# Performance work log

Measured on AMD Instinct MI355X. Metric: run time of the kernel, lower is better.

The kernel has to match this reference:

```python
import jax, jax.numpy as jnp
import numpy as np
from jax import lax

BASE_SIZE = 16.0
FEAT_STRIDE = 16
RATIOS = (0.5, 1.0, 2.0)
SCALES = (8.0, 16.0, 32.0)
N_PRE_NMS = 6000   # eval-mode ProposalCreator defaults
N_POST_NMS = 300
NMS_THRESH = 0.7
MIN_SIZE = 16.0
SCALE = 1.0


def anchor_base():
    # generate_anchor_base: loops ratio-major, scale-minor -> 9 anchors (y1,x1,y2,x2)
    r = jnp.asarray(RATIOS, jnp.float32)
    s = jnp.asarray(SCALES, jnp.float32)
    h = (BASE_SIZE * s[None, :] * jnp.sqrt(r)[:, None]).reshape(-1)
    w = (BASE_SIZE * s[None, :] * jnp.sqrt(1.0 / r)[:, None]).reshape(-1)
    c = BASE_SIZE / 2.0
    return jnp.stack([c - h / 2, c - w / 2, c + h / 2, c + w / 2], axis=1)  # [9,4]


def enumerate_anchors(hh, ww):
    # replicates _enumerate_shift_anchor incl. torch.meshgrid(shift_x, shift_y) 'ij' ordering
    sy = jnp.arange(hh, dtype=jnp.float32) * FEAT_STRIDE
    sx = jnp.arange(ww, dtype=jnp.float32) * FEAT_STRIDE
    gx, gy = jnp.meshgrid(sx, sy, indexing='ij')  # shapes [ww, hh]
    shift = jnp.stack([gy.ravel(), gx.ravel(), gy.ravel(), gx.ravel()], axis=1)  # [K,4]
    a = anchor_base()[None, :, :] + shift[:, None, :]  # [K,9,4]
    return a.reshape(-1, 4)


def conv2d(x, w, b, pad):
    y = lax.conv_general_dilated(x, w, (1, 1), [(pad, pad), (pad, pad)],
                                 dimension_numbers=('NCHW', 'OIHW', 'NCHW'))
    return y + b[None, :, None, None]


def loc2bbox(anchor, loc):
    h = anchor[:, 2] - anchor[:, 0]
    w = anchor[:, 3] - anchor[:, 1]
    cy = anchor[:, 0] + 0.5 * h
    cx = anchor[:, 1] + 0.5 * w
    dy, dx, dh, dw = loc[:, 0], loc[:, 1], loc[:, 2], loc[:, 3]
    cy = dy * h + cy
    cx = dx * w + cx
    h = jnp.exp(dh) * h
    w = jnp.exp(dw) * w
    return jnp.stack([cy - 0.5 * h, cx - 0.5 * w, cy + 0.5 * h, cx + 0.5 * w], axis=1)


def propose(loc, score, anchor, img_h, img_w):
    # ProposalCreator for a single image: decode, clip, min-size filter, top-k, NMS, pad to N_POST_NMS
    roi = loc2bbox(anchor, loc)
    roi = jnp.stack([jnp.clip(roi[:, 0], 0.0, img_h), jnp.clip(roi[:, 1], 0.0, img_w),
                     jnp.clip(roi[:, 2], 0.0, img_h), jnp.clip(roi[:, 3], 0.0, img_w)], axis=1)
    ms = MIN_SIZE * SCALE
    valid = ((roi[:, 2] - roi[:, 0]) >= ms) & ((roi[:, 3] - roi[:, 1]) >= ms)
    score = jnp.where(valid, score, -jnp.inf)
    top_s, order = lax.top_k(score, N_PRE_NMS)          # score-descending candidates
    boxes = roi[order]                                   # [N_PRE,4]
    valid_s = top_s > -jnp.inf
    # pairwise IoU [N_PRE,N_PRE]
    area = (boxes[:, 2] - boxes[:, 0]) * (boxes[:, 3] - boxes[:, 1])
    tl = jnp.maximum(boxes[:, None, :2], boxes[None, :, :2])
    br = jnp.minimum(boxes[:, None, 2:], boxes[None, :, 2:])
    inter = jnp.prod(jnp.clip(br - tl, 0.0, None), axis=-1)
    iou = lax.stop_gradient(inter / (area[:, None] + area[None, :] - inter))
    idxs = jnp.arange(N_PRE_NMS)
    def body(keep, i):
        sup = (iou[i] > NMS_THRESH) & (idxs > i) & keep[i]
        return keep & ~sup, None
    keep, _ = lax.scan(body, valid_s, idxs)              # greedy NMS over score-sorted boxes
    # kept indices in score order (stable argsort: True(kept) sorts first as 0)
    sel = jnp.argsort(jnp.logical_not(keep))[:N_POST_NMS]
    out_valid = jnp.arange(N_POST_NMS) < jnp.sum(keep)
    return jnp.where(out_valid[:, None], boxes[sel], 0.0)  # [N_POST,4], zero-padded


def rpn_forward(x, conv1_w, conv1_b, score_w, score_b, loc_w, loc_b, img_h, img_w):
    n, _, hh, ww = x.shape
    anchor = enumerate_anchors(hh, ww)                   # [hh*ww*9, 4]
    A = anchor.shape[0] // (hh * ww)
    feat = jax.nn.relu(conv2d(x, conv1_w, conv1_b, 1))   # [n,512,hh,ww]
    locs = conv2d(feat, loc_w, loc_b, 0).transpose(0, 2, 3, 1).reshape(n, -1, 4)
    raw_scores = conv2d(feat, score_w, score_b, 0).transpose(0, 2, 3, 1)  # [n,hh,ww,A*2]
    fg = jax.nn.softmax(raw_scores.reshape(n, hh, ww, A, 2), axis=4)[..., 1].reshape(n, -1)
    scores = raw_scores.reshape(n, -1, 2)
    rois = jax.vmap(lambda l, s: propose(l, s, anchor, float(img_h), float(img_w)))(locs, fg)
    roi_indices = jnp.broadcast_to(jnp.arange(n, dtype=jnp.int32)[:, None], (n, N_POST_NMS))
    return locs, scores, rois, roi_indices, anchor


def setup_inputs() -> dict:
    key = jax.random.key(0)
    ks = jax.random.split(key, 4)
    x = jax.random.normal(ks[0], (4, 512, 50, 50), jnp.float32)
    conv1_w = jax.random.normal(ks[1], (512, 512, 3, 3), jnp.float32) * 0.01
    conv1_b = jnp.zeros((512,), jnp.float32)
    score_w = jax.random.normal(ks[2], (18, 512, 1, 1), jnp.float32) * 0.01
    score_b = jnp.zeros((18,), jnp.float32)
    loc_w = jax.random.normal(ks[3], (36, 512, 1, 1), jnp.float32) * 0.01
    loc_b = jnp.zeros((36,), jnp.float32)
    return {'x': x, 'conv1_w': conv1_w, 'conv1_b': conv1_b, 'score_w': score_w,
            'score_b': score_b, 'loc_w': loc_w, 'loc_b': loc_b, 'img_h': 800, 'img_w': 800}


def reference(x, conv1_w, conv1_b, score_w, score_b, loc_w, loc_b, img_h, img_w):
    return rpn_forward(x, conv1_w, conv1_b, score_w, score_b, loc_w, loc_b, img_h, img_w)
```

## Files before the change

### kernel.cpp

```cpp
#include <hip/hip_runtime.h>
#include <stdint.h>

#define NB 4
#define CIN 512
#define PIX 2500
#define KTOT 4608
#define NBOX 22500
#define NPRE 6000
#define NPOST 300
#define NWORD 94
#define SCAP 8192

#define O_LOCS   0
#define O_SCORES 360000
#define O_ROIS   540000
#define O_RIDX   544800
#define O_ANCH   546000

#define XT_ROWS 2960
#define XT_FRONT 64
#define XT_IMG (XT_ROWS * 512)
#define XT_SPLIT_BYTES ((size_t)NB * XT_IMG * 2)

#define WO_XT1   0ull
#define WO_XT2   12124160ull
#define WO_WSBLK 24248320ull
#define WO_FEATP 33685504ull
#define WO_WT    74645504ull
#define WO_BOXES 74760192ull
#define WO_DKEY  76200192ull
#define WO_BOX6K 76560192ull
#define WO_VALID 76944192ull
#define WO_MASK  0ull

#define FEATP_HALF 5120000

typedef _Float16 h8 __attribute__((ext_vector_type(8)));
typedef float f32x4 __attribute__((ext_vector_type(4)));
typedef unsigned int u32;
typedef unsigned long long u64;

__device__ __forceinline__ void gll16(const void* g, void* l) {
  __builtin_amdgcn_global_load_lds((const __attribute__((address_space(1))) u32*)g,
                                   (__attribute__((address_space(3))) u32*)l, 16, 0, 0);
}

__device__ __forceinline__ float rd_dim(const int* p) {
  int v = *p;
  if (v > 0 && v < 1000000) return (float)v;
  return __int_as_float(v);
}

__global__ void k_zero(u32* __restrict__ xt) {
  size_t n = (2 * XT_SPLIT_BYTES) / 4;
  for (size_t i = blockIdx.x * 256ull + threadIdx.x; i < n; i += (size_t)gridDim.x * 256)
    xt[i] = 0u;
}

__global__ void k_xT(const float* __restrict__ x, _Float16* __restrict__ x1,
                     _Float16* __restrict__ x2) {
  __shared__ float sx[3200];
  int chunk = blockIdx.x, r0 = blockIdx.y, b = blockIdx.z;
  int t = threadIdx.x;
  int ic0 = chunk * 64;
  for (int i = t; i < 3200; i += 256) {
    int icl = i / 50, c = i - icl * 50;
    sx[i] = x[(((size_t)b * 512 + ic0 + icl) * 50 + r0) * 50 + c];
  }
  __syncthreads();
  for (int j = t; j < 3200; j += 256) {
    int c = j >> 6, icl = j & 63;
    float v = sx[icl * 50 + c];
    _Float16 h1 = (_Float16)v;
    _Float16 h2 = (_Float16)(v - (float)h1);
    size_t dst = (size_t)b * XT_IMG + (size_t)(XT_FRONT + (r0 + 1) * 52 + (c + 1)) * 512 + ic0 + icl;
    x1[dst] = h1;
    x2[dst] = h2;
  }
}

__global__ void k_splitw(const float* __restrict__ w, _Float16* __restrict__ wblk) {
  int n = 4 * 144 * 16 * 512;
  for (int idx = blockIdx.x * 256 + threadIdx.x; idx < n; idx += gridDim.x * 256) {
    int lane8 = idx & 511;
    int l = lane8 >> 3, j = lane8 & 7;
    int reg = (idx >> 9) & 15;
    int t = idx >> 13;
    int ksI = t % 144, mt = t / 144;
    int ocs = reg >> 1, s = reg & 1;
    int oc = mt * 128 + ocs * 16 + (l & 15);
    int k = ksI * 32 + (l >> 4) * 8 + j;
    int tap = k >> 9, ic = k & 511;
    float v = w[((size_t)oc * 512 + ic) * 9 + tap];
    _Float16 h1 = (_Float16)v;
    wblk[idx] = s ? (_Float16)(v - (float)h1) : h1;
  }
}

__global__ void k_wt(const float* __restrict__ loc_w, const float* __restrict__ score_w,
                     float* __restrict__ wt) {
  int idx = blockIdx.x * 256 + threadIdx.x;
  if (idx >= 128 * 56 * 4) return;
  int i = idx & 3, j = (idx >> 2) % 56, c4 = idx / 224;
  int c = c4 * 4 + i;
  float v = 0.f;
  if (j < 36) v = loc_w[(size_t)j * 512 + c];
  else if (j < 54) v = score_w[(size_t)(j - 36) * 512 + c];
  wt[idx] = v;
}

__global__ __launch_bounds__(128, 2) void k_conv(
    const _Float16* __restrict__ xs1, const _Float16* __restrict__ xs2,
    const _Float16* __restrict__ wsBlk,
    float* __restrict__ featP) {
  __shared__ _Float16 lds[8192];
  int id = blockIdx.x;
  int bz = id & 7;
  int inner = id >> 3;
  int st = inner / 88;
  int idx2 = inner - st * 88;
  int nt = idx2 >> 1;
  int mt = st * 2 + (idx2 & 1);
  int b = bz >> 1, ks = bz & 1;
  int t = threadIdx.x, lane = t & 63, w = t >> 6;
  int mb = mt * 128, nb = nt * 64;
  int l15 = lane & 15, l4 = lane >> 4;
  const _Float16* xi1 = xs1 + (size_t)b * XT_IMG + (size_t)XT_FRONT * 512;
  const _Float16* xi2 = xs2 + (size_t)b * XT_IMG + (size_t)XT_FRONT * 512;
  const _Float16* wbase = wsBlk + ((size_t)(mt * 144 + ks * 72) * 16 + w * 8) * 512 + lane * 8;

  f32x4 acc[4][4];
#pragma unroll
  for (int i = 0; i < 4; i++)
#pragma unroll
    for (int j = 0; j < 4; j++)
      acc[i][j] = (f32x4){0.f, 0.f, 0.f, 0.f};

  auto stageB = [&](int kk, int off) {
    int kg = ks * 2304 + kk * 32;
    int tap = kg >> 9, ic0 = kg & 511;
    int sh = (tap / 3 - 1) * 52 + (tap % 3) - 1;
#pragma unroll
    for (int u = 0; u < 4; u++) {
      int r = w * 4 + u;
      int pxs = r >> 1, s = r & 1;
      const _Float16* xp = s ? xi2 : xi1;
      int qp = nb + pxs * 16 + l15 + sh;
      gll16(xp + (ptrdiff_t)qp * 512 + ic0 + l4 * 8, &lds[off + r * 512]);
    }
  };
  auto loadA = [&](int kk, h8* a) {
    const _Float16* p = wbase + (size_t)kk * 16 * 512;
#pragma unroll
    for (int u = 0; u < 8; u++) a[u] = *(const h8*)(p + u * 512);
  };
  auto compute = [&](int off, const h8* a) {
#pragma unroll
    for (int nf = 0; nf < 4; nf++) {
      h8 b0 = *(const h8*)&lds[off + (nf * 2 + 0) * 512 + lane * 8];
      h8 b1 = *(const h8*)&lds[off + (nf * 2 + 1) * 512 + lane * 8];
      __builtin_amdgcn_s_setprio(1);
#pragma unroll
      for (int mf = 0; mf < 4; mf++) {
        acc[mf][nf] = __builtin_amdgcn_mfma_f32_16x16x32_f16(a[mf * 2 + 0], b0, acc[mf][nf], 0, 0, 0);
        acc[mf][nf] = __builtin_amdgcn_mfma_f32_16x16x32_f16(a[mf * 2 + 0], b1, acc[mf][nf], 0, 0, 0);
        acc[mf][nf] = __builtin_amdgcn_mfma_f32_16x16x32_f16(a[mf * 2 + 1], b0, acc[mf][nf], 0, 0, 0);
      }
      __builtin_amdgcn_s_setprio(0);
    }
  };

  h8 aA[8], aB[8];
  loadA(0, aA);
  stageB(0, 0);
  __syncthreads();
#pragma unroll 1
  for (int kp = 0; kp < 36; kp++) {
    int kk = 2 * kp;
    stageB(kk + 1, 4096);
    loadA(kk + 1, aB);
    compute(0, aA);
    __syncthreads();
    if (kp < 35) {
      stageB(kk + 2, 0);
      loadA(kk + 2, aA);
    }
    compute(4096, aB);
    __syncthreads();
  }

  float* fp = featP + (size_t)ks * FEATP_HALF;
#pragma unroll
  for (int nf = 0; nf < 4; nf++) {
    int q = nb + nf * 16 + l15;
    int r = q / 52, c = q - r * 52;
    if (r >= 1 && r <= 50 && c >= 1 && c <= 50) {
      int p = (r - 1) * 50 + (c - 1);
      size_t base = ((size_t)b * PIX + p) * 512;
#pragma unroll
      for (int mf = 0; mf < 4; mf++) {
        int oc0 = mb + w * 64 + mf * 16 + l4 * 4;
        *(float4*)&fp[base + oc0] = make_float4(acc[mf][nf][0], acc[mf][nf][1],
                                                acc[mf][nf][2], acc[mf][nf][3]);
      }
    }
  }
}

__global__ __launch_bounds__(256) void k_heads(const float* __restrict__ featP,
                                               const float* __restrict__ wt4,
                                               const float* __restrict__ conv_b,
                                               const float* __restrict__ loc_b,
                                               const float* __restrict__ score_b,
                                               const int* __restrict__ ihp,
                                               const int* __restrict__ iwp,
                                               float* __restrict__ out,
                                               float* __restrict__ boxes,
                                               uint32_t* __restrict__ dkey) {
  int wid = blockIdx.x * 4 + (threadIdx.x >> 6);
  if (wid >= NB * PIX) return;
  int lane = threadIdx.x & 63;
  int b = wid / PIX, p = wid % PIX;
  int row = lane < 54 ? lane : 54;
  const float* f0 = featP + ((size_t)b * PIX + p) * 512;
  const float* f1 = f0 + FEATP_HALF;
  float acc = 0.f;
  for (int c4 = 0; c4 < 128; c4++) {
    float4 u = *(const float4*)(f0 + c4 * 4);
    float4 v = *(const float4*)(f1 + c4 * 4);
    float4 bb = *(const float4*)(conv_b + c4 * 4);
    float4 wv = *(const float4*)(wt4 + ((size_t)c4 * 56 + row) * 4);
    acc += fmaxf(u.x + v.x + bb.x, 0.f) * wv.x;
    acc += fmaxf(u.y + v.y + bb.y, 0.f) * wv.y;
    acc += fmaxf(u.z + v.z + bb.z, 0.f) * wv.z;
    acc += fmaxf(u.w + v.w + bb.w, 0.f) * wv.w;
  }
  float bi = 0.f;
  if (lane < 36) bi = loc_b[lane];
  else if (lane < 54) bi = score_b[lane - 36];
  acc += bi;
  if (lane < 36) out[O_LOCS + (size_t)b * 90000 + (size_t)p * 36 + lane] = acc;
  else if (lane < 54) out[O_SCORES + (size_t)b * 45000 + (size_t)p * 18 + (lane - 36)] = acc;

  float imgH = rd_dim(ihp), imgW = rd_dim(iwp);
  int gy = p % 50, gx = p / 50;
  float sy = 16.f * gy, sx = 16.f * gx;

  int a9 = (lane < 9) ? lane : 0;
  float dy  = __shfl(acc, a9 * 4 + 0);
  float dxv = __shfl(acc, a9 * 4 + 1);
  float dh  = __shfl(acc, a9 * 4 + 2);
  float dw  = __shfl(acc, a9 * 4 + 3);
  float l0  = __shfl(acc, 36 + a9 * 2);
  float l1  = __shfl(acc, 36 + a9 * 2 + 1);

  {
    float rr = (a9 < 3) ? 0.5f : (a9 < 6 ? 1.f : 2.f);
    int si = a9 % 3;
    float ssc = (si == 0) ? 8.f : (si == 1 ? 16.f : 32.f);
    float hb = 16.f * ssc * sqrtf(rr);
    float wb = 16.f * ssc * sqrtf(1.f / rr);
    float ay1 = (8.f - hb * 0.5f) + sy;
    float ax1 = (8.f - wb * 0.5f) + sx;
    float ay2 = (8.f + hb * 0.5f) + sy;
    float ax2 = (8.f + wb * 0.5f) + sx;
    float h = ay2 - ay1, w2d = ax2 - ax1;
    float cy = ay1 + 0.5f * h, cx = ax1 + 0.5f * w2d;
    float cy2 = dy * h + cy, cx2 = dxv * w2d + cx;
    float h2 = expf(dh) * h, ww2 = expf(dw) * w2d;
    float y1 = cy2 - 0.5f * h2, x1 = cx2 - 0.5f * ww2;
    float y2 = cy2 + 0.5f * h2, x2 = cx2 + 0.5f * ww2;
    y1 = fminf(fmaxf(y1, 0.f), imgH);
    x1 = fminf(fmaxf(x1, 0.f), imgW);
    y2 = fminf(fmaxf(y2, 0.f), imgH);
    x2 = fminf(fmaxf(x2, 0.f), imgW);
    bool valid = (y2 - y1 >= 16.f) && (x2 - x1 >= 16.f);
    float m = fmaxf(l0, l1);
    float e0 = expf(l0 - m), e1 = expf(l1 - m);
    float fg = e1 / (e0 + e1);
    float scv = valid ? fg : -INFINITY;
    if (lane < 9) {
      size_t k = (size_t)b * NBOX + (size_t)p * 9 + a9;
      *(float4*)(boxes + k * 4) = make_float4(y1, x1, y2, x2);
      uint32_t u = __float_as_uint(scv);
      uint32_t f2 = (u >> 31) ? ~u : (u | 0x80000000u);
      dkey[k] = ~f2;
    }
  }
  if (b == 0 && lane < 36) {
    int aa = lane >> 2, dd = lane & 3;
    float rr2 = (aa < 3) ? 0.5f : (aa < 6 ? 1.f : 2.f);
    int si2 = aa % 3;
    float ss2 = (si2 == 0) ? 8.f : (si2 == 1 ? 16.f : 32.f);
    float hb2 = 16.f * ss2 * sqrtf(rr2);
    float wb2 = 16.f * ss2 * sqrtf(1.f / rr2);
    float v;
    if (dd == 0) v = (8.f - hb2 * 0.5f) + sy;
    else if (dd == 1) v = (8.f - wb2 * 0.5f) + sx;
    else if (dd == 2) v = (8.f + hb2 * 0.5f) + sy;
    else v = (8.f + wb2 * 0.5f) + sx;
    out[O_ANCH + (size_t)p * 36 + lane] = v;
  }
}

__global__ void k_topk(const uint32_t* __restrict__ dkey, const float* __restrict__ boxes,
                       float* __restrict__ box6k,
                       unsigned long long* __restrict__ validm) {
  extern __shared__ char smem[];
  u64* cand = (u64*)smem;
  u64* alt  = (u64*)(smem + 65536);
  u32* hcnt = (u32*)(smem + 131072);
  u32* wc     = (u32*)(smem + 139264);
  u32* digTot = wc + 16;
  u32* digBase = digTot + 16;
  u32* msc = digBase + 16;
  u32* histw = (u32*)(smem + 65536);
  u32* hist = histw + 4096;
  int b = blockIdx.x, tid = threadIdx.x;
  int wq = tid >> 6, l = tid & 63;
  const uint32_t* dk = dkey + (size_t)b * NBOX;

  uint32_t P = 0, need = NPRE;
  for (int pass = 0; pass < 4; pass++) {
    int sh = 24 - 8 * pass;
    for (int i = tid; i < 16 * 256; i += 1024) histw[i] = 0;
    __syncthreads();
    for (int i = tid; i < NBOX; i += 1024) {
      uint32_t d = dk[i];
      bool match = (((uint64_t)d >> (sh + 8)) == ((uint64_t)P >> (sh + 8)));
      if (match) atomicAdd(&histw[wq * 256 + ((d >> sh) & 255u)], 1u);
    }
    __syncthreads();
    for (int bin = tid; bin < 256; bin += 1024) {
      uint32_t s = 0;
#pragma unroll
      for (int q = 0; q < 16; q++) s += histw[q * 256 + bin];
      hist[bin] = s;
    }
    __syncthreads();
    if (tid < 64) {
      uint32_t h0 = hist[l * 4 + 0], h1 = hist[l * 4 + 1];
      uint32_t h2 = hist[l * 4 + 2], h3 = hist[l * 4 + 3];
      uint32_t p1 = h0, p2 = h0 + h1, p3 = p2 + h2, p4 = p3 + h3;
      uint32_t s = p4;
#pragma unroll
      for (int dd = 1; dd < 64; dd <<= 1) { uint32_t v = __shfl_up(s, dd); if (l >= dd) s += v; }
      uint32_t excl = s - p4;
      uint32_t i0 = excl + p1, i1 = excl + p2, i2 = excl + p3, i3 = excl + p4;
      int local = 4;
      if (i0 >= need) local = 0;
      else if (i1 >= need) local = 1;
      else if (i2 >= need) local = 2;
      else if (i3 >= need) local = 3;
      u64 bal = __ballot(local < 4);
      int lw = bal ? __builtin_ctzll(bal) : 63;
      if (l == lw) {
        if (local < 4) {
          msc[0] = (uint32_t)(l * 4 + local);
          msc[1] = (local == 0) ? excl : (local == 1) ? i0 : (local == 2) ? i1 : i2;
        } else {
          msc[0] = 255u;
          msc[1] = i2;
        }
      }
    }
    __syncthreads();
    need -= msc[1];
    P |= msc[0] << sh;
    __syncthreads();
  }
  uint32_t Dstar = P;

  if (tid == 0) msc[2] = 0;
  __syncthreads();
  for (int c = 0; c < 22; c++) {
    int i = c * 1024 + tid;
    uint32_t d = (i < NBOX) ? dk[i] : 0xFFFFFFFFu;
    bool pred = (i < NBOX) && (d <= Dstar);
    u64 bal = __ballot(pred);
    uint32_t rank = (uint32_t)__popcll(bal & ((1ull << l) - 1ull));
    __syncthreads();
    if (l == 0) wc[wq] = (uint32_t)__popcll(bal);
    __syncthreads();
    if (tid < 64) {
      uint32_t v = (l < 16) ? wc[l] : 0u;
      uint32_t s = v;
#pragma unroll
      for (int dd = 1; dd < 16; dd <<= 1) { uint32_t t2 = __shfl_up(s, dd); if (l >= dd) s += t2; }
      uint32_t base0 = msc[2];
      if (l < 16) wc[l] = base0 + s - v;
      if (l == 15) msc[2] = base0 + s;
    }
    __syncthreads();
    if (pred) {
      uint32_t pos = wc[wq] + rank;
      if (pos < SCAP) cand[pos] = ((u64)d << 32) | (uint32_t)i;
    }
  }
  __syncthreads();
  uint32_t cnt = msc[2] < SCAP ? msc[2] : SCAP;
  for (int i = (int)cnt + tid; i < SCAP; i += 1024) cand[i] = ~0ull;
  __syncthreads();

  u64* src = cand;
  u64* dst = alt;
  for (int pass = 0; pass < 8; pass++) {
    int sh = 32 + pass * 4;
    for (int i = tid; i < 2048; i += 1024) hcnt[i] = 0;
    __syncthreads();
    for (int c = 0; c < 8; c++) {
      int i = c * 1024 + tid;
      uint32_t dig = (uint32_t)(src[i] >> sh) & 15u;
      u64 m = ~0ull;
#pragma unroll
      for (int bit = 0; bit < 4; bit++) {
        u64 bb = __ballot((dig >> bit) & 1u);
        m &= ((dig >> bit) & 1u) ? bb : ~bb;
      }
      if (l == __builtin_ctzll(m)) hcnt[(i >> 6) * 16 + dig] = (uint32_t)__popcll(m);
    }
    __syncthreads();
    {
      int d = wq;
      uint32_t cl = hcnt[l * 16 + d];
      uint32_t ch = hcnt[(l + 64) * 16 + d];
      uint32_t s = cl;
#pragma unroll
      for (int dd = 1; dd < 64; dd <<= 1) { uint32_t v = __shfl_up(s, dd); if (l >= dd) s += v; }
      uint32_t tl = __shfl(s, 63);
      uint32_t el = s - cl;
      uint32_t s2 = ch;
#pragma unroll
      for (int dd = 1; dd < 64; dd <<= 1) { uint32_t v = __shfl_up(s2, dd); if (l >= dd) s2 += v; }
      uint32_t th = __shfl(s2, 63);
      uint32_t eh = tl + (s2 - ch);
      hcnt[l * 16 + d] = el;
      hcnt[(l + 64) * 16 + d] = eh;
      if (l == 0) digTot[d] = tl + th;
    }
    __syncthreads();
    if (tid == 0) {
      uint32_t basev = 0;
      for (int d2 = 0; d2 < 16; d2++) { digBase[d2] = basev; basev += digTot[d2]; }
    }
    __syncthreads();
    for (int c = 0; c < 8; c++) {
      int i = c * 1024 + tid;
      u64 key = src[i];
      uint32_t dig = (uint32_t)(key >> sh) & 15u;
      u64 m = ~0ull;
#pragma unroll
      for (int bit = 0; bit < 4; bit++) {
        u64 bb = __ballot((dig >> bit) & 1u);
        m &= ((dig >> bit) & 1u) ? bb : ~bb;
      }
      uint32_t rank = (uint32_t)__popcll(m & ((1ull << l) - 1ull));
      uint32_t dpos = digBase[dig] + hcnt[(i >> 6) * 16 + dig] + rank;
      dst[dpos] = key;
    }
    __syncthreads();
    u64* tmp = src; src = dst; dst = tmp;
  }

  for (int r = tid; r < NPRE; r += 1024) {
    u64 kk = cand[r];
    uint32_t idx = (uint32_t)kk;
    float4 bx = *(const float4*)(boxes + ((size_t)b * NBOX + idx) * 4);
    *(float4*)(box6k + ((size_t)b * NPRE + r) * 4) = bx;
  }
  for (int wi = tid; wi < NWORD; wi += 1024) {
    unsigned long long m = 0ull;
    for (int bb = 0; bb < 64; bb++) {
      int r = wi * 64 + bb;
      if (r < NPRE) {
        uint32_t d = (uint32_t)(cand[r] >> 32);
        if (d < 0xFF800000u) m |= (1ull << bb);
      }
    }
    validm[b * NWORD + wi] = m;
  }
}

__global__ __launch_bounds__(256) void k_mask(const float* __restrict__ box6k,
                                              unsigned long long* __restrict__ mask) {
  int b = blockIdx.z, it = blockIdx.x, wt = blockIdx.y;
  int t = threadIdx.x;
  int il = t & 31, wl = t >> 5;
  if (wt * 512 + 511 <= it * 32) return;
  __shared__ float bi[32][4];
  __shared__ float bj[512][4];
  if (t < 128) {
    int ii = it * 32 + (t >> 2);
    if (ii > NPRE - 1) ii = NPRE - 1;
    bi[t >> 2][t & 3] = box6k[((size_t)b * NPRE + ii) * 4 + (t & 3)];
  }
#pragma unroll
  for (int q = 0; q < 2; q++) {
    int v = t + 256 * q;
    int jg = wt * 512 + v;
    float4 f = make_float4(0.f, 0.f, 0.f, 0.f);
    if (jg < NPRE) f = *(const float4*)(box6k + ((size_t)b * NPRE + jg) * 4);
    *(float4*)&bj[v][0] = f;
  }
  __syncthreads();
  int i = it * 32 + il;
  int w = wt * 8 + wl;
  if (i >= NPRE || w >= NWORD) return;
  float y1 = bi[il][0], x1 = bi[il][1], y2 = bi[il][2], x2 = bi[il][3];
  float ar = (y2 - y1) * (x2 - x1);
  unsigned long long m = 0ull;
  int jbase = w * 64;
  for (int jj = 0; jj < 64; jj++) {
    int j = jbase + jj;
    int js = wl * 64 + jj;
    float jy1 = bj[js][0], jx1 = bj[js][1], jy2 = bj[js][2], jx2 = bj[js][3];
    float tlY = fmaxf(y1, jy1), tlX = fmaxf(x1, jx1);
    float brY = fminf(y2, jy2), brX = fminf(x2, jx2);
    float ih = fmaxf(brY - tlY, 0.f), iw2 = fmaxf(brX - tlX, 0.f);
    float inter = ih * iw2;
    float arj = (jy2 - jy1) * (jx2 - jx1);
    float iou = inter / (ar + arj - inter);
    if (iou > 0.7f && j > i && j < NPRE) m |= (1ull << jj);
  }
  mask[((size_t)b * NPRE + i) * NWORD + w] = m;
}

__global__ void k_scan(const unsigned long long* __restrict__ mask,
                       const unsigned long long* __restrict__ validm,
                       const float* __restrict__ box6k, float* __restrict__ out) {
  int b = blockIdx.x;
  int lane = threadIdx.x;
  const unsigned long long* mb = mask + (size_t)b * NPRE * NWORD;
  u64 a0 = (lane < NWORD) ? validm[b * NWORD + lane] : 0ull;
  u64 a1 = (lane + 64 < NWORD) ? validm[b * NWORD + lane + 64] : 0ull;
  __shared__ int keptIdx[NPOST];
  int cnt = 0;
  bool done = false;
  u64 rowCur = mb[(size_t)lane * NWORD + 0];
  for (int w = 0; w < NWORD && !done; w++) {
    u64 rowNext = 0ull;
    if (w + 1 < NWORD) {
      int i2 = (w + 1) * 64 + lane;
      if (i2 < NPRE) rowNext = mb[(size_t)i2 * NWORD + (w + 1)];
    }
    u64 alive = (w < 64) ? __shfl(a0, w) : __shfl(a1, w - 64);
    if (alive) {
      u64 keep = 0ull;
      while (alive) {
        int q = __builtin_ctzll(alive);
        alive &= alive - 1;
        keep |= (1ull << q);
        if (lane == 0) keptIdx[cnt] = w * 64 + q;
        cnt++;
        if (cnt >= NPOST) { done = true; break; }
        alive &= ~__shfl(rowCur, q);
      }
      if (w < 64) { if (lane == w) a0 = 0ull; }
      else        { if (lane == w - 64) a1 = 0ull; }
      if (!done) {
        while (keep) {
          u64 or0 = 0ull, or1 = 0ull;
#pragma unroll
          for (int z = 0; z < 8; z++) {
            if (keep) {
              int q = __builtin_ctzll(keep);
              keep &= keep - 1;
              int ki = w * 64 + q;
              u64 m0 = (lane < NWORD && lane > w) ? mb[(size_t)ki * NWORD + lane] : 0ull;
              u64 m1 = (lane + 64 < NWORD && lane + 64 > w) ? mb[(size_t)ki * NWORD + 64 + lane] : 0ull;
              or0 |= m0;
              or1 |= m1;
            }
          }
          a0 &= ~or0;
          a1 &= ~or1;
        }
      }
    }
    rowCur = rowNext;
  }
  __syncthreads();
  for (int r = lane; r < NPOST; r += 64) {
    float4 bx = make_float4(0.f, 0.f, 0.f, 0.f);
    if (r < cnt) bx = *(const float4*)(box6k + ((size_t)b * NPRE + keptIdx[r]) * 4);
    *(float4*)(out + O_ROIS + ((size_t)b * NPOST + r) * 4) = bx;
    out[O_RIDX + b * NPOST + r] = (float)b;
  }
}

extern "C" void kernel_launch(void* const* d_in, const int* in_sizes, int n_in,
                              void* d_out, int out_size, void* d_ws, size_t ws_size,
                              hipStream_t stream) {
  const float* x       = (const float*)d_in[0];
  const float* conv1_w = (const float*)d_in[1];
  const float* conv1_b = (const float*)d_in[2];
  const float* score_w = (const float*)d_in[3];
  const float* score_b = (const float*)d_in[4];
  const float* loc_w   = (const float*)d_in[5];
  const float* loc_b   = (const float*)d_in[6];
  const int* ihp = (const int*)d_in[7];
  const int* iwp = (const int*)d_in[8];
  float* out = (float*)d_out;
  char* ws = (char*)d_ws;
  _Float16* xt1 = (_Float16*)(ws + WO_XT1);
  _Float16* xt2 = (_Float16*)(ws + WO_XT2);
  _Float16* wsBlk = (_Float16*)(ws + WO_WSBLK);
  float* featP = (float*)(ws + WO_FEATP);
  float* wt    = (float*)(ws + WO_WT);
  float* boxes = (float*)(ws + WO_BOXES);
  uint32_t* dkey  = (uint32_t*)(ws + WO_DKEY);
  float* box6k = (float*)(ws + WO_BOX6K);
  unsigned long long* validm = (unsigned long long*)(ws + WO_VALID);
  unsigned long long* mask   = (unsigned long long*)(ws + WO_MASK);

  k_zero<<<2048, 256, 0, stream>>>((u32*)xt1);
  k_xT<<<dim3(8, 50, NB), 256, 0, stream>>>(x, xt1, xt2);
  k_splitw<<<2048, 256, 0, stream>>>(conv1_w, wsBlk);
  k_wt<<<(128 * 56 * 4 + 255) / 256, 256, 0, stream>>>(loc_w, score_w, wt);
  k_conv<<<1408, 128, 0, stream>>>(xt1, xt2, wsBlk, featP);
  k_heads<<<(NB * PIX + 3) / 4, 256, 0, stream>>>(featP, wt, conv1_b, loc_b, score_b,
                                                  ihp, iwp, out, boxes, dkey);
  int topk_lds = 65536 * 2 + 8192 + 512;
  hipFuncSetAttribute((const void*)k_topk, hipFuncAttributeMaxDynamicSharedMemorySize,
                      topk_lds);
  k_topk<<<NB, 1024, topk_lds, stream>>>(dkey, boxes, box6k, validm);
  dim3 gm(188, 12, NB);
  k_mask<<<gm, 256, 0, stream>>>(box6k, mask);
  k_scan<<<NB, 64, 0, stream>>>(mask, validm, box6k, out);
}
```

Baseline: 607.7 us.

## Triple-buffer conv K-loop with explicit vmcnt waits and raw barriers

Replaces the double-buffered main loop of the implicit-GEMM conv with a three-stage ring of LDS B tiles and A register sets. Manual s_waitcnt vmcnt and s_barrier calls, fenced by sched_barrier, keep two tiles of global loads in flight while the current one is computed. The aim is to hide more global-load latency behind MFMA work. In exchange it uses more LDS and more VGPRs for the third A buffer, which may lower occupancy. Correctness now depends on the hand-counted vmcnt values matching the actual number of loads issued per stage.

```diff
diff --git a/kernel.cpp b/kernel.cpp
--- a/kernel.cpp
+++ b/kernel.cpp
@@ -109,11 +109,13 @@
   wt[idx] = v;
 }
 
+#define VMW20 asm volatile("s_waitcnt vmcnt(20)" ::: "memory")
+#define VMW8  asm volatile("s_waitcnt vmcnt(8)" ::: "memory")
 __global__ __launch_bounds__(128, 2) void k_conv(
     const _Float16* __restrict__ xs1, const _Float16* __restrict__ xs2,
     const _Float16* __restrict__ wsBlk,
     float* __restrict__ featP) {
-  __shared__ _Float16 lds[8192];
+  __shared__ _Float16 lds[12288];
   int id = blockIdx.x;
   int bz = id & 7;
   int inner = id >> 3;
@@ -170,24 +172,42 @@
     }
   };
 
-  h8 aA[8], aB[8];
-  loadA(0, aA);
+  h8 a0[8], a1[8], a2[8];
   stageB(0, 0);
-  __syncthreads();
+  loadA(0, a0);
+  stageB(1, 4096);
+  loadA(1, a1);
+
 #pragma unroll 1
-  for (int kp = 0; kp < 36; kp++) {
-    int kk = 2 * kp;
-    stageB(kk + 1, 4096);
-    loadA(kk + 1, aB);
-    compute(0, aA);
-    __syncthreads();
-    if (kp < 35) {
-      stageB(kk + 2, 0);
-      loadA(kk + 2, aA);
-    }
-    compute(4096, aB);
-    __syncthreads();
-  }
+  for (int kp = 0; kp < 23; kp++) {
+    int kk = 3 * kp;
+    VMW20; __builtin_amdgcn_sched_barrier(0);
+    __builtin_amdgcn_s_barrier(); __builtin_amdgcn_sched_barrier(0);
+    stageB(kk + 2, 8192);
+    loadA(kk + 2, a2);
+    compute(0, a0);
+    VMW20; __builtin_amdgcn_sched_barrier(0);
+    __builtin_amdgcn_s_barrier(); __builtin_amdgcn_sched_barrier(0);
+    stageB(kk + 3, 0);
+    loadA(kk + 3, a0);
+    compute(4096, a1);
+    VMW20; __builtin_amdgcn_sched_barrier(0);
+    __builtin_amdgcn_s_barrier(); __builtin_amdgcn_sched_barrier(0);
+    stageB(kk + 4, 4096);
+    loadA(kk + 4, a1);
+    compute(8192, a2);
+  }
+  VMW20; __builtin_amdgcn_sched_barrier(0);
+  __builtin_amdgcn_s_barrier(); __builtin_amdgcn_sched_barrier(0);
+  stageB(71, 8192);
+  loadA(71, a2);
+  compute(0, a0);
+  VMW20; __builtin_amdgcn_sched_barrier(0);
+  __builtin_amdgcn_s_barrier(); __builtin_amdgcn_sched_barrier(0);
+  compute(4096, a1);
+  VMW8; __builtin_amdgcn_sched_barrier(0);
+  __builtin_amdgcn_s_barrier(); __builtin_amdgcn_sched_barrier(0);
+  compute(8192, a2);
 
   float* fp = featP + (size_t)ks * FEATP_HALF;
 #pragma unroll
```

New measurement: 638.3 us. +5.0%, slower.

## Enlarge conv N-tile to 128 and replace full NMS mask with lazy in-LDS NMS

Applied to the files above, without the earlier changes.

The conv kernel's pixel tile is doubled from 64 to 128 per block, which doubles the LDS staging buffer and the accumulator registers and halves the grid to 704 blocks. This raises reuse of the weight fragments per B tile, at the cost of more register pressure and fewer blocks in flight. The precomputed 6000x94 IoU bitmask and the separate scan kernel are replaced by a single per-image NMS kernel. That kernel keeps all boxes in LDS and computes IoU only for the current 64-box word and for suppression by kept boxes. It stops once 300 boxes are kept, so it avoids the large mask write and read, but it serialises the work onto one workgroup per image.

```diff
diff --git a/kernel.cpp b/kernel.cpp
--- a/kernel.cpp
+++ b/kernel.cpp
@@ -31,7 +31,6 @@
 #define WO_DKEY  76200192ull
 #define WO_BOX6K 76560192ull
 #define WO_VALID 76944192ull
-#define WO_MASK  0ull
 
 #define FEATP_HALF 5120000
 
@@ -113,27 +112,27 @@
     const _Float16* __restrict__ xs1, const _Float16* __restrict__ xs2,
     const _Float16* __restrict__ wsBlk,
     float* __restrict__ featP) {
-  __shared__ _Float16 lds[8192];
+  __shared__ _Float16 lds[16384];
   int id = blockIdx.x;
   int bz = id & 7;
   int inner = id >> 3;
-  int st = inner / 88;
-  int idx2 = inner - st * 88;
+  int st = inner / 44;
+  int idx2 = inner - st * 44;
   int nt = idx2 >> 1;
   int mt = st * 2 + (idx2 & 1);
   int b = bz >> 1, ks = bz & 1;
   int t = threadIdx.x, lane = t & 63, w = t >> 6;
-  int mb = mt * 128, nb = nt * 64;
+  int mb = mt * 128, nb = nt * 128;
   int l15 = lane & 15, l4 = lane >> 4;
   const _Float16* xi1 = xs1 + (size_t)b * XT_IMG + (size_t)XT_FRONT * 512;
   const _Float16* xi2 = xs2 + (size_t)b * XT_IMG + (size_t)XT_FRONT * 512;
   const _Float16* wbase = wsBlk + ((size_t)(mt * 144 + ks * 72) * 16 + w * 8) * 512 + lane * 8;
 
-  f32x4 acc[4][4];
+  f32x4 acc[4][8];
 #pragma unroll
   for (int i = 0; i < 4; i++)
 #pragma unroll
-    for (int j = 0; j < 4; j++)
+    for (int j = 0; j < 8; j++)
       acc[i][j] = (f32x4){0.f, 0.f, 0.f, 0.f};
 
   auto stageB = [&](int kk, int off) {
@@ -141,8 +140,8 @@
     int tap = kg >> 9, ic0 = kg & 511;
     int sh = (tap / 3 - 1) * 52 + (tap % 3) - 1;
 #pragma unroll
-    for (int u = 0; u < 4; u++) {
-      int r = w * 4 + u;
+    for (int u = 0; u < 8; u++) {
+      int r = w * 8 + u;
       int pxs = r >> 1, s = r & 1;
       const _Float16* xp = s ? xi2 : xi1;
       int qp = nb + pxs * 16 + l15 + sh;
@@ -156,7 +155,7 @@
   };
   auto compute = [&](int off, const h8* a) {
 #pragma unroll
-    for (int nf = 0; nf < 4; nf++) {
+    for (int nf = 0; nf < 8; nf++) {
       h8 b0 = *(const h8*)&lds[off + (nf * 2 + 0) * 512 + lane * 8];
       h8 b1 = *(const h8*)&lds[off + (nf * 2 + 1) * 512 + lane * 8];
       __builtin_amdgcn_s_setprio(1);
@@ -177,7 +176,7 @@
 #pragma unroll 1
   for (int kp = 0; kp < 36; kp++) {
     int kk = 2 * kp;
-    stageB(kk + 1, 4096);
+    stageB(kk + 1, 8192);
     loadA(kk + 1, aB);
     compute(0, aA);
     __syncthreads();
@@ -185,13 +184,13 @@
       stageB(kk + 2, 0);
       loadA(kk + 2, aA);
     }
-    compute(4096, aB);
+    compute(8192, aB);
     __syncthreads();
   }
 
   float* fp = featP + (size_t)ks * FEATP_HALF;
 #pragma unroll
-  for (int nf = 0; nf < 4; nf++) {
+  for (int nf = 0; nf < 8; nf++) {
     int q = nb + nf * 16 + l15;
     int r = q / 52, c = q - r * 52;
     if (r >= 1 && r <= 50 && c >= 1 && c <= 50) {
@@ -481,109 +480,106 @@
   }
 }
 
-__global__ __launch_bounds__(256) void k_mask(const float* __restrict__ box6k,
-                                              unsigned long long* __restrict__ mask) {
-  int b = blockIdx.z, it = blockIdx.x, wt = blockIdx.y;
-  int t = threadIdx.x;
-  int il = t & 31, wl = t >> 5;
-  if (wt * 512 + 511 <= it * 32) return;
-  __shared__ float bi[32][4];
-  __shared__ float bj[512][4];
-  if (t < 128) {
-    int ii = it * 32 + (t >> 2);
-    if (ii > NPRE - 1) ii = NPRE - 1;
-    bi[t >> 2][t & 3] = box6k[((size_t)b * NPRE + ii) * 4 + (t & 3)];
-  }
-#pragma unroll
-  for (int q = 0; q < 2; q++) {
-    int v = t + 256 * q;
-    int jg = wt * 512 + v;
-    float4 f = make_float4(0.f, 0.f, 0.f, 0.f);
-    if (jg < NPRE) f = *(const float4*)(box6k + ((size_t)b * NPRE + jg) * 4);
-    *(float4*)&bj[v][0] = f;
-  }
+#define NMS_BX   0
+#define NMS_ROWS 96000
+#define NMS_AVL  96512
+#define NMS_KIDX 97264
+#define NMS_SCAL 98464
+#define NMS_KM   98472
+#define NMS_LDS  98480
+__global__ void k_nms(const float* __restrict__ box6k,
+                      const unsigned long long* __restrict__ validm,
+                      float* __restrict__ out) {
+  extern __shared__ char sm[];
+  float4* bx = (float4*)(sm + NMS_BX);
+  u64* rows = (u64*)(sm + NMS_ROWS);
+  u64* avail = (u64*)(sm + NMS_AVL);
+  int* keptIdx = (int*)(sm + NMS_KIDX);
+  int* scal = (int*)(sm + NMS_SCAL);
+  u64* km = (u64*)(sm + NMS_KM);
+  int b = blockIdx.x, tid = threadIdx.x;
+  int wv = tid >> 6, l = tid & 63;
+  for (int i = tid; i < NPRE; i += 1024)
+    bx[i] = *(const float4*)(box6k + ((size_t)b * NPRE + i) * 4);
+  for (int i = tid; i < NWORD; i += 1024) avail[i] = validm[b * NWORD + i];
+  if (tid == 0) { scal[0] = 0; scal[1] = 0; }
   __syncthreads();
-  int i = it * 32 + il;
-  int w = wt * 8 + wl;
-  if (i >= NPRE || w >= NWORD) return;
-  float y1 = bi[il][0], x1 = bi[il][1], y2 = bi[il][2], x2 = bi[il][3];
-  float ar = (y2 - y1) * (x2 - x1);
-  unsigned long long m = 0ull;
-  int jbase = w * 64;
-  for (int jj = 0; jj < 64; jj++) {
-    int j = jbase + jj;
-    int js = wl * 64 + jj;
-    float jy1 = bj[js][0], jx1 = bj[js][1], jy2 = bj[js][2], jx2 = bj[js][3];
-    float tlY = fmaxf(y1, jy1), tlX = fmaxf(x1, jx1);
-    float brY = fminf(y2, jy2), brX = fminf(x2, jx2);
-    float ih = fmaxf(brY - tlY, 0.f), iw2 = fmaxf(brX - tlX, 0.f);
-    float inter = ih * iw2;
-    float arj = (jy2 - jy1) * (jx2 - jx1);
-    float iou = inter / (ar + arj - inter);
-    if (iou > 0.7f && j > i && j < NPRE) m |= (1ull << jj);
-  }
-  mask[((size_t)b * NPRE + i) * NWORD + w] = m;
-}
-
-__global__ void k_scan(const unsigned long long* __restrict__ mask,
-                       const unsigned long long* __restrict__ validm,
-                       const float* __restrict__ box6k, float* __restrict__ out) {
-  int b = blockIdx.x;
-  int lane = threadIdx.x;
-  const unsigned long long* mb = mask + (size_t)b * NPRE * NWORD;
-  u64 a0 = (lane < NWORD) ? validm[b * NWORD + lane] : 0ull;
-  u64 a1 = (lane + 64 < NWORD) ? validm[b * NWORD + lane + 64] : 0ull;
-  __shared__ int keptIdx[NPOST];
-  int cnt = 0;
-  bool done = false;
-  u64 rowCur = mb[(size_t)lane * NWORD + 0];
-  for (int w = 0; w < NWORD && !done; w++) {
-    u64 rowNext = 0ull;
-    if (w + 1 < NWORD) {
-      int i2 = (w + 1) * 64 + lane;
-      if (i2 < NPRE) rowNext = mb[(size_t)i2 * NWORD + (w + 1)];
-    }
-    u64 alive = (w < 64) ? __shfl(a0, w) : __shfl(a1, w - 64);
-    if (alive) {
+  for (int w = 0; w < NWORD; w++) {
+    u64 alive = avail[w];
+    if (alive == 0ull) continue;
+    int base = w * 64;
+#pragma unroll
+    for (int rr = 0; rr < 4; rr++) {
+      int r = wv * 4 + rr;
+      int ci = base + r, cj = base + l;
+      float4 bi4 = bx[ci < NPRE ? ci : NPRE - 1];
+      float4 bj4 = bx[cj < NPRE ? cj : NPRE - 1];
+      float ari = (bi4.z - bi4.x) * (bi4.w - bi4.y);
+      float arj = (bj4.z - bj4.x) * (bj4.w - bj4.y);
+      float tlY = fmaxf(bi4.x, bj4.x), tlX = fmaxf(bi4.y, bj4.y);
+      float brY = fminf(bi4.z, bj4.z), brX = fminf(bi4.w, bj4.w);
+      float ih = fmaxf(brY - tlY, 0.f), iw2 = fmaxf(brX - tlX, 0.f);
+      float inter = ih * iw2;
+      float iou = inter / (ari + arj - inter);
+      bool sup = (iou > 0.7f) && (l > r) && (cj < NPRE);
+      u64 bal = __ballot(sup);
+      if (l == 0) rows[r] = bal;
+    }
+    __syncthreads();
+    if (tid < 64) {
+      u64 rowL = rows[l];
       u64 keep = 0ull;
-      while (alive) {
-        int q = __builtin_ctzll(alive);
-        alive &= alive - 1;
+      int cnt = scal[0];
+      bool done = false;
+      u64 aw = alive;
+      while (aw) {
+        int q = __builtin_ctzll(aw);
+        aw &= aw - 1;
         keep |= (1ull << q);
-        if (lane == 0) keptIdx[cnt] = w * 64 + q;
+        if (l == 0) keptIdx[cnt] = base + q;
         cnt++;
         if (cnt >= NPOST) { done = true; break; }
-        alive &= ~__shfl(rowCur, q);
-      }
-      if (w < 64) { if (lane == w) a0 = 0ull; }
-      else        { if (lane == w - 64) a1 = 0ull; }
-      if (!done) {
-        while (keep) {
-          u64 or0 = 0ull, or1 = 0ull;
-#pragma unroll
-          for (int z = 0; z < 8; z++) {
-            if (keep) {
-              int q = __builtin_ctzll(keep);
-              keep &= keep - 1;
-              int ki = w * 64 + q;
-              u64 m0 = (lane < NWORD && lane > w) ? mb[(size_t)ki * NWORD + lane] : 0ull;
-              u64 m1 = (lane + 64 < NWORD && lane + 64 > w) ? mb[(size_t)ki * NWORD + 64 + lane] : 0ull;
-              or0 |= m0;
-              or1 |= m1;
-            }
-          }
-          a0 &= ~or0;
-          a1 &= ~or1;
-        }
-      }
-    }
-    rowCur = rowNext;
+        aw &= ~__shfl(rowL, q);
+      }
+      if (l == 0) {
+        scal[0] = cnt;
+        scal[1] = done ? 1 : 0;
+        km[0] = keep;
+        avail[w] = 0ull;
+      }
+    }
+    __syncthreads();
+    if (scal[1]) break;
+    u64 keep = km[0];
+    for (int tw = w + 1 + wv; tw < NWORD; tw += 16) {
+      int c = tw * 64 + l;
+      float4 cb = bx[c < NPRE ? c : NPRE - 1];
+      float arc = (cb.z - cb.x) * (cb.w - cb.y);
+      bool supAny = false;
+      u64 kk = keep;
+      while (kk) {
+        int q = __builtin_ctzll(kk);
+        kk &= kk - 1;
+        float4 kb = bx[base + q];
+        float ark = (kb.z - kb.x) * (kb.w - kb.y);
+        float tlY = fmaxf(kb.x, cb.x), tlX = fmaxf(kb.y, cb.y);
+        float brY = fminf(kb.z, cb.z), brX = fminf(kb.w, cb.w);
+        float ih = fmaxf(brY - tlY, 0.f), iw2 = fmaxf(brX - tlX, 0.f);
+        float inter = ih * iw2;
+        float iou = inter / (ark + arc - inter);
+        supAny |= (iou > 0.7f);
+      }
+      u64 bal = __ballot(supAny && (c < NPRE));
+      if (l == 0) avail[tw] &= ~bal;
+    }
+    __syncthreads();
   }
   __syncthreads();
-  for (int r = lane; r < NPOST; r += 64) {
-    float4 bx = make_float4(0.f, 0.f, 0.f, 0.f);
-    if (r < cnt) bx = *(const float4*)(box6k + ((size_t)b * NPRE + keptIdx[r]) * 4);
-    *(float4*)(out + O_ROIS + ((size_t)b * NPOST + r) * 4) = bx;
+  int cnt = scal[0];
+  for (int r = tid; r < NPOST; r += 1024) {
+    float4 bo = make_float4(0.f, 0.f, 0.f, 0.f);
+    if (r < cnt) bo = bx[keptIdx[r]];
+    *(float4*)(out + O_ROIS + ((size_t)b * NPOST + r) * 4) = bo;
     out[O_RIDX + b * NPOST + r] = (float)b;
   }
 }
@@ -611,20 +607,19 @@
   uint32_t* dkey  = (uint32_t*)(ws + WO_DKEY);
   float* box6k = (float*)(ws + WO_BOX6K);
   unsigned long long* validm = (unsigned long long*)(ws + WO_VALID);
-  unsigned long long* mask   = (unsigned long long*)(ws + WO_MASK);
 
   k_zero<<<2048, 256, 0, stream>>>((u32*)xt1);
   k_xT<<<dim3(8, 50, NB), 256, 0, stream>>>(x, xt1, xt2);
   k_splitw<<<2048, 256, 0, stream>>>(conv1_w, wsBlk);
   k_wt<<<(128 * 56 * 4 + 255) / 256, 256, 0, stream>>>(loc_w, score_w, wt);
-  k_conv<<<1408, 128, 0, stream>>>(xt1, xt2, wsBlk, featP);
+  k_conv<<<704, 128, 0, stream>>>(xt1, xt2, wsBlk, featP);
   k_heads<<<(NB * PIX + 3) / 4, 256, 0, stream>>>(featP, wt, conv1_b, loc_b, score_b,
                                                   ihp, iwp, out, boxes, dkey);
   int topk_lds = 65536 * 2 + 8192 + 512;
   hipFuncSetAttribute((const void*)k_topk, hipFuncAttributeMaxDynamicSharedMemorySize,
                       topk_lds);
   k_topk<<<NB, 1024, topk_lds, stream>>>(dkey, boxes, box6k, validm);
-  dim3 gm(188, 12, NB);
-  k_mask<<<gm, 256, 0, stream>>>(box6k, mask);
-  k_scan<<<NB, 64, 0, stream>>>(mask, validm, box6k, out);
-}
+  hipFuncSetAttribute((const void*)k_nms, hipFuncAttributeMaxDynamicSharedMemorySize,
+                      NMS_LDS);
+  k_nms<<<NB, 1024, NMS_LDS, stream>>>(box6k, validm, out);
+}
```

After: 825.3 us. +35.8%, slower.

## Load conv B fragments directly into registers and deepen NMS scan row prefetch

Applied to the files above, without the earlier changes.

The conv kernel no longer stages activation tiles through LDS with global_load_lds and barriers. Each wave now loads its B fragments straight from global memory into registers, double-buffered alongside the A fragments, and the setprio hints are dropped. This removes LDS traffic and both __syncthreads per iteration, at the cost of more VGPRs and redundant global loads across waves. The NMS scan kernel also prefetches diagonal mask rows two words ahead instead of one, to hide load latency.

```diff
diff --git a/kernel.cpp b/kernel.cpp
--- a/kernel.cpp
+++ b/kernel.cpp
@@ -39,11 +39,6 @@
 typedef float f32x4 __attribute__((ext_vector_type(4)));
 typedef unsigned int u32;
 typedef unsigned long long u64;
-
-__device__ __forceinline__ void gll16(const void* g, void* l) {
-  __builtin_amdgcn_global_load_lds((const __attribute__((address_space(1))) u32*)g,
-                                   (__attribute__((address_space(3))) u32*)l, 16, 0, 0);
-}
 
 __device__ __forceinline__ float rd_dim(const int* p) {
   int v = *p;
@@ -113,7 +108,6 @@
     const _Float16* __restrict__ xs1, const _Float16* __restrict__ xs2,
     const _Float16* __restrict__ wsBlk,
     float* __restrict__ featP) {
-  __shared__ _Float16 lds[8192];
   int id = blockIdx.x;
   int bz = id & 7;
   int inner = id >> 3;
@@ -123,7 +117,7 @@
   int mt = st * 2 + (idx2 & 1);
   int b = bz >> 1, ks = bz & 1;
   int t = threadIdx.x, lane = t & 63, w = t >> 6;
-  int mb = mt * 128, nb = nt * 64;
+  int nb = nt * 64;
   int l15 = lane & 15, l4 = lane >> 4;
   const _Float16* xi1 = xs1 + (size_t)b * XT_IMG + (size_t)XT_FRONT * 512;
   const _Float16* xi2 = xs2 + (size_t)b * XT_IMG + (size_t)XT_FRONT * 512;
@@ -136,57 +130,49 @@
     for (int j = 0; j < 4; j++)
       acc[i][j] = (f32x4){0.f, 0.f, 0.f, 0.f};
 
-  auto stageB = [&](int kk, int off) {
+  auto loadA = [&](int kk, h8* a) {
+    const _Float16* p = wbase + (size_t)kk * 16 * 512;
+#pragma unroll
+    for (int u = 0; u < 8; u++) a[u] = *(const h8*)(p + u * 512);
+  };
+  auto loadB = [&](int kk, h8* bf) {
     int kg = ks * 2304 + kk * 32;
     int tap = kg >> 9, ic0 = kg & 511;
     int sh = (tap / 3 - 1) * 52 + (tap % 3) - 1;
 #pragma unroll
-    for (int u = 0; u < 4; u++) {
-      int r = w * 4 + u;
-      int pxs = r >> 1, s = r & 1;
-      const _Float16* xp = s ? xi2 : xi1;
-      int qp = nb + pxs * 16 + l15 + sh;
-      gll16(xp + (ptrdiff_t)qp * 512 + ic0 + l4 * 8, &lds[off + r * 512]);
+    for (int nf = 0; nf < 4; nf++) {
+      ptrdiff_t off = (ptrdiff_t)(nb + nf * 16 + l15 + sh) * 512 + ic0 + l4 * 8;
+      bf[nf * 2 + 0] = *(const h8*)(xi1 + off);
+      bf[nf * 2 + 1] = *(const h8*)(xi2 + off);
     }
   };
-  auto loadA = [&](int kk, h8* a) {
-    const _Float16* p = wbase + (size_t)kk * 16 * 512;
-#pragma unroll
-    for (int u = 0; u < 8; u++) a[u] = *(const h8*)(p + u * 512);
-  };
-  auto compute = [&](int off, const h8* a) {
+  auto compute = [&](const h8* a, const h8* bf) {
 #pragma unroll
     for (int nf = 0; nf < 4; nf++) {
-      h8 b0 = *(const h8*)&lds[off + (nf * 2 + 0) * 512 + lane * 8];
-      h8 b1 = *(const h8*)&lds[off + (nf * 2 + 1) * 512 + lane * 8];
-      __builtin_amdgcn_s_setprio(1);
+      h8 b0 = bf[nf * 2 + 0], b1 = bf[nf * 2 + 1];
 #pragma unroll
       for (int mf = 0; mf < 4; mf++) {
         acc[mf][nf] = __builtin_amdgcn_mfma_f32_16x16x32_f16(a[mf * 2 + 0], b0, acc[mf][nf], 0, 0, 0);
         acc[mf][nf] = __builtin_amdgcn_mfma_f32_16x16x32_f16(a[mf * 2 + 0], b1, acc[mf][nf], 0, 0, 0);
         acc[mf][nf] = __builtin_amdgcn_mfma_f32_16x16x32_f16(a[mf * 2 + 1], b0, acc[mf][nf], 0, 0, 0);
       }
-      __builtin_amdgcn_s_setprio(0);
     }
   };
 
-  h8 aA[8], aB[8];
+  h8 aA[8], bA[8], aB[8], bB[8];
   loadA(0, aA);
-  stageB(0, 0);
-  __syncthreads();
+  loadB(0, bA);
 #pragma unroll 1
   for (int kp = 0; kp < 36; kp++) {
     int kk = 2 * kp;
-    stageB(kk + 1, 4096);
     loadA(kk + 1, aB);
-    compute(0, aA);
-    __syncthreads();
+    loadB(kk + 1, bB);
+    compute(aA, bA);
     if (kp < 35) {
-      stageB(kk + 2, 0);
       loadA(kk + 2, aA);
-    }
-    compute(4096, aB);
-    __syncthreads();
+      loadB(kk + 2, bA);
+    }
+    compute(aB, bB);
   }
 
   float* fp = featP + (size_t)ks * FEATP_HALF;
@@ -199,7 +185,7 @@
       size_t base = ((size_t)b * PIX + p) * 512;
 #pragma unroll
       for (int mf = 0; mf < 4; mf++) {
-        int oc0 = mb + w * 64 + mf * 16 + l4 * 4;
+        int oc0 = mt * 128 + w * 64 + mf * 16 + l4 * 4;
         *(float4*)&fp[base + oc0] = make_float4(acc[mf][nf][0], acc[mf][nf][1],
                                                 acc[mf][nf][2], acc[mf][nf][3]);
       }
@@ -537,11 +523,12 @@
   int cnt = 0;
   bool done = false;
   u64 rowCur = mb[(size_t)lane * NWORD + 0];
+  u64 rowN1 = mb[(size_t)(64 + lane) * NWORD + 1];
   for (int w = 0; w < NWORD && !done; w++) {
-    u64 rowNext = 0ull;
-    if (w + 1 < NWORD) {
-      int i2 = (w + 1) * 64 + lane;
-      if (i2 < NPRE) rowNext = mb[(size_t)i2 * NWORD + (w + 1)];
+    u64 rowN2 = 0ull;
+    if (w + 2 < NWORD) {
+      int i2 = (w + 2) * 64 + lane;
+      if (i2 < NPRE) rowN2 = mb[(size_t)i2 * NWORD + (w + 2)];
     }
     u64 alive = (w < 64) ? __shfl(a0, w) : __shfl(a1, w - 64);
     if (alive) {
@@ -577,7 +564,8 @@
         }
       }
     }
-    rowCur = rowNext;
+    rowCur = rowN1;
+    rowN1 = rowN2;
   }
   __syncthreads();
   for (int r = lane; r < NPOST; r += 64) {
```

Result: slower. 688.4 us (+13.3%).
